# Optimization experiments

Measured on AMD Instinct MI355X. Metric: run time of the kernel, lower is better.

## Reference

```python
import jax, jax.numpy as jnp
import numpy as np

EPS = 1e-5
K_PATCHES = 5000  # sample_pixels // 16


def _resize_bilinear(x, h, w):
    # matches torch F.interpolate(mode='bilinear', align_corners=False)
    return jax.image.resize(x, (x.shape[0], x.shape[1], h, w), method="bilinear", antialias=False)


def _bn(x, g, b, m, v):
    # eval-mode BatchNorm2d with running stats
    inv = jax.lax.rsqrt(v + EPS)
    return (x - m[None, :, None, None]) * (g * inv)[None, :, None, None] + b[None, :, None, None]


def _conv(x, w):
    return jax.lax.conv_general_dilated(x, w, (1, 1), "VALID",
                                        dimension_numbers=("NCHW", "OIHW", "NCHW"))


def setup_inputs():
    key = jax.random.key(0)
    ks = jax.random.split(key, 14)
    B, Hc, Wc = 2, 512, 512
    pha = jax.random.uniform(ks[0], (B, 1, Hc, Wc), jnp.float32)
    err = jax.random.uniform(ks[1], (B, 1, Hc, Wc), jnp.float32)  # strictly >0 so mask is all-ones
    hid = jax.random.normal(ks[2], (B, 32, Hc, Wc), jnp.float32)

    def conv_w(k, o, i):
        return jax.random.normal(k, (o, i, 3, 3), jnp.float32) * 0.05

    def bn_p(k, c):
        k1, k2 = jax.random.split(k)
        return (1.0 + 0.1 * jax.random.normal(k1, (c,), jnp.float32),
                0.1 * jax.random.normal(k2, (c,), jnp.float32),
                jnp.zeros((c,), jnp.float32), jnp.ones((c,), jnp.float32))

    g1, b1, m1, v1 = bn_p(ks[4], 24)
    g2, b2, m2, v2 = bn_p(ks[6], 16)
    g3, b3, m3, v3 = bn_p(ks[8], 12)
    return dict(pha=pha, err=err, hid=hid,
                w1=conv_w(ks[3], 24, 33), g1=g1, b1=b1, m1=m1, v1=v1,
                w2=conv_w(ks[5], 16, 24), g2=g2, b2=b2, m2=m2, v2=v2,
                w3=conv_w(ks[7], 12, 16), g3=g3, b3=b3, m3=m3, v3=v3,
                w4=conv_w(ks[9], 1, 12),
                b4=0.1 * jax.random.normal(ks[10], (1,), jnp.float32),
                H_full=2048, W_full=2048)


def reference(pha, err, hid, w1, g1, b1, m1, v1, w2, g2, b2, m2, v2,
              w3, g3, b3, m3, v3, w4, b4, H_full, W_full):
    B = pha.shape[0]
    Hh, Wh = H_full // 2, W_full // 2
    Hq, Wq = H_full // 4, W_full // 4

    # --- select_refinement_regions (sampling mode) ---
    err_q = _resize_bilinear(err, Hq, Wq)                      # (B,1,Hq,Wq)
    flat = err_q.reshape(B, -1)
    _, top_idx = jax.lax.top_k(flat, K_PATCHES)                # (B,K)
    ref = jnp.zeros_like(flat).at[jnp.arange(B)[:, None], top_idx].set(1.0)
    ref = ref * (flat > 0).astype(flat.dtype)                  # prevent_oversampling
    ref = ref.reshape(B, 1, Hq, Wq)

    # nonzero(ref) == topk locations here (err is strictly positive)
    bidx = jnp.repeat(jnp.arange(B), K_PATCHES)                # (P,)
    hidx = (top_idx // Wq).reshape(-1)                         # (P,)
    widx = (top_idx % Wq).reshape(-1)                          # (P,)

    # --- crop_patch (unfold-equivalent gather), size=2, padding=3 ---
    x = jnp.concatenate([hid, pha], axis=1)                    # (B,33,Hc,Wc)
    x = _resize_bilinear(x, Hh, Wh)                            # (B,33,Hh,Wh)
    pad, size = 3, 2
    win = size + 2 * pad                                       # 8
    xp = jnp.pad(x, ((0, 0), (0, 0), (pad, pad), (pad, pad)))
    rows = hidx[:, None] * size + jnp.arange(win)              # (P,8)
    cols = widx[:, None] * size + jnp.arange(win)              # (P,8)
    patches = xp[bidx[:, None, None], :, rows[:, :, None], cols[:, None, :]]  # (P,8,8,33)
    patches = patches.transpose(0, 3, 1, 2)                    # (P,33,8,8)

    # --- small conv stack ---
    y = jax.nn.relu(_bn(_conv(patches, w1), g1, b1, m1, v1))   # (P,24,6,6)
    y = jax.nn.relu(_bn(_conv(y, w2), g2, b2, m2, v2))         # (P,16,4,4)
    y = jnp.repeat(jnp.repeat(y, 2, axis=2), 2, axis=3)        # nearest -> (P,16,8,8)
    y = jax.nn.relu(_bn(_conv(y, w3), g3, b3, m3, v3))         # (P,12,6,6)
    y = _conv(y, w4) + b4[None, :, None, None]                 # (P,1,4,4)

    # --- replace_patch (scatter_nd of 4x4 blocks into full-res pha) ---
    pha_full = _resize_bilinear(pha, H_full, W_full)           # (B,1,H,W)
    pr = hidx[:, None, None] * 4 + jnp.arange(4)[None, :, None]  # (P,4,1)
    pc = widx[:, None, None] * 4 + jnp.arange(4)[None, None, :]  # (P,1,4)
    pha_full = pha_full.at[bidx[:, None, None], 0, pr, pc].set(y[:, 0])
    return pha_full, ref
```

## Files before the change

### kernel.cpp

```cpp
#include <hip/hip_runtime.h>
#include <stdint.h>

#define K_SEL 5000
#define NQ    262144
#define NB    2

#define BIAS_OFF 38912
#define W4_OFF   39424
#define ST_OFF   40960
#define XT_OFF   135168
#define XT_BYTES ((size_t)NB * NQ * 40 * 2)
#define WS_NEED  (XT_OFF + XT_BYTES)

#define WS_HIST  16
#define WS_SEL   2064
#define WS_EQ    12064
#define EQ_CAP   4096
#define WS_BCNT  20480
#define WS_BBASE 21504

typedef _Float16 f16x8 __attribute__((ext_vector_type(8)));
typedef _Float16 f16x4 __attribute__((ext_vector_type(4)));
typedef float    f32x4 __attribute__((ext_vector_type(4)));
#define MFMA16(a,b,c) __builtin_amdgcn_mfma_f32_16x16x32_f16(a,b,c,0,0,0)

__global__ void prep_kernel(const float* __restrict__ w1, const float* __restrict__ g1,
                            const float* __restrict__ b1, const float* __restrict__ m1,
                            const float* __restrict__ v1,
                            const float* __restrict__ w2, const float* __restrict__ g2,
                            const float* __restrict__ b2, const float* __restrict__ m2,
                            const float* __restrict__ v2,
                            const float* __restrict__ w3, const float* __restrict__ g3,
                            const float* __restrict__ b3, const float* __restrict__ m3,
                            const float* __restrict__ v3,
                            const float* __restrict__ w4, const float* __restrict__ b4,
                            char* __restrict__ ws) {
    _Float16* wf = (_Float16*)ws;
    float* bias = (float*)(ws + BIAS_OFF);
    float* w4r  = (float*)(ws + W4_OFF);
    uint32_t* st = (uint32_t*)(ws + ST_OFF);
    int tid = threadIdx.x;
    for (int t = tid; t < 38 * 512; t += 256) {
        int frag = t >> 9, li = (t >> 3) & 63, j = t & 7;
        int lo = li & 15, hi = li >> 4;
        float val = 0.f;
        if (frag < 18) {
            int ky = frag / 6, r = frag % 6, kx = r >> 1, mt = r & 1;
            int oc = mt * 16 + lo, ci = hi * 8 + j;
            if (oc < 24) val = w1[((oc * 33 + ci) * 3 + ky) * 3 + kx] * g1[oc] * rsqrtf(v1[oc] + 1e-5f);
        } else if (frag < 27) {
            int f = frag - 18, ky = f / 3, kt = f % 3;
            int oc = lo, k = kt * 32 + hi * 8 + j;
            if (k < 72) {
                int kx = k / 24, ci = k % 24;
                val = w2[((oc * 24 + ci) * 3 + ky) * 3 + kx] * g2[oc] * rsqrtf(v2[oc] + 1e-5f);
            }
        } else if (frag < 36) {
            int s = frag - 27, ky = s / 3, kx = s % 3;
            int oc = lo, ci = hi * 8 + j;
            if (oc < 12 && ci < 16) val = w3[((oc * 16 + ci) * 3 + ky) * 3 + kx] * g3[oc] * rsqrtf(v3[oc] + 1e-5f);
        } else {
            int mt = frag - 36, oc = mt * 16 + lo, tap = hi * 8 + j;
            if (oc < 24 && tap < 9)
                val = w1[((oc * 33 + 32) * 3 + tap / 3) * 3 + tap % 3] * g1[oc] * rsqrtf(v1[oc] + 1e-5f);
        }
        wf[t] = (_Float16)val;
    }
    if (tid < 53) {
        float v;
        if (tid < 24)      { float sc = g1[tid] * rsqrtf(v1[tid] + 1e-5f); v = b1[tid] - m1[tid] * sc; }
        else if (tid < 40) { int c = tid - 24; float sc = g2[c] * rsqrtf(v2[c] + 1e-5f); v = b2[c] - m2[c] * sc; }
        else if (tid < 52) { int c = tid - 40; float sc = g3[c] * rsqrtf(v3[c] + 1e-5f); v = b3[c] - m3[c] * sc; }
        else v = b4[0];
        bias[tid] = v;
    }
    if (tid < 144) { int t9 = tid / 16, ci = tid % 16; w4r[tid] = (ci < 12) ? w4[ci * 9 + t9] : 0.f; }
    for (int i = tid; i < WS_HIST + 4 * 512; i += 256) st[i] = 0u;
    __syncthreads();
    if (tid == 0) { st[2] = K_SEL; st[3] = K_SEL; }
}

__device__ __forceinline__ void tu_work(int tb, const float* __restrict__ hid,
                                        const float* __restrict__ pha,
                                        _Float16* __restrict__ xt,
                                        float* __restrict__ out) {
    int tid = threadIdx.x;
    if (tb < 2048) {
        int t = tb * 256 + tid;
        int b = t >> 18, i = t & (NQ - 1);
        _Float16 v[40];
#pragma unroll
        for (int c = 0; c < 32; c++)
            v[c] = (_Float16)hid[((size_t)(b * 32 + c)) * NQ + i];
        v[32] = (_Float16)pha[(size_t)b * NQ + i];
#pragma unroll
        for (int c = 33; c < 40; c++) v[c] = (_Float16)0.f;
        _Float16* dst = xt + (size_t)t * 40;
#pragma unroll
        for (int q = 0; q < 5; q++) *(f16x8*)(dst + q * 8) = *(const f16x8*)(v + q * 8);
    } else {
        int t = (tb - 2048) * 256 + tid;
        int xq = t & 511;
        int rest = t >> 9;
        int oy = rest & 2047;
        int b  = rest >> 11;
        const float* src = pha + (size_t)b * NQ;
        float sy = oy * 0.25f - 0.375f;
        sy = fminf(fmaxf(sy, 0.0f), 511.0f);
        int y0 = (int)sy; int y1i = min(y0 + 1, 511);
        float fy = sy - (float)y0;
        float rv[4];
#pragma unroll
        for (int j = 0; j < 4; j++) {
            int ox = xq * 4 + j;
            float sx = ox * 0.25f - 0.375f;
            sx = fminf(fmaxf(sx, 0.0f), 511.0f);
            int x0 = (int)sx; int x1i = min(x0 + 1, 511);
            float fx = sx - (float)x0;
            float v00 = src[y0 * 512 + x0],  v01 = src[y0 * 512 + x1i];
            float v10 = src[y1i * 512 + x0], v11 = src[y1i * 512 + x1i];
            rv[j] = v00 * (1.f - fy) * (1.f - fx) + v01 * (1.f - fy) * fx
                  + v10 * fy * (1.f - fx)         + v11 * fy * fx;
        }
        float4 r4 = make_float4(rv[0], rv[1], rv[2], rv[3]);
        *reinterpret_cast<float4*>(out + (size_t)b * 4194304 + (size_t)oy * 2048 + xq * 4) = r4;
    }
}

__global__ void upsample_kernel(const float* __restrict__ pha, float* __restrict__ out) {
    int t = blockIdx.x * 256 + threadIdx.x;
    int xq = t & 511;
    int rest = t >> 9;
    int oy = rest & 2047;
    int b  = rest >> 11;
    const float* src = pha + (size_t)b * NQ;
    float sy = oy * 0.25f - 0.375f;
    sy = fminf(fmaxf(sy, 0.0f), 511.0f);
    int y0 = (int)sy; int y1i = min(y0 + 1, 511);
    float fy = sy - (float)y0;
    float rv[4];
#pragma unroll
    for (int j = 0; j < 4; j++) {
        int ox = xq * 4 + j;
        float sx = ox * 0.25f - 0.375f;
        sx = fminf(fmaxf(sx, 0.0f), 511.0f);
        int x0 = (int)sx; int x1i = min(x0 + 1, 511);
        float fx = sx - (float)x0;
        float v00 = src[y0 * 512 + x0],  v01 = src[y0 * 512 + x1i];
        float v10 = src[y1i * 512 + x0], v11 = src[y1i * 512 + x1i];
        rv[j] = v00 * (1.f - fy) * (1.f - fx) + v01 * (1.f - fy) * fx
              + v10 * fy * (1.f - fx)         + v11 * fy * fx;
    }
    float4 r4 = make_float4(rv[0], rv[1], rv[2], rv[3]);
    *reinterpret_cast<float4*>(out + (size_t)b * 4194304 + (size_t)oy * 2048 + xq * 4) = r4;
}

__global__ void hist_kernel(const float* __restrict__ err, uint32_t* st, int round,
                            const float* __restrict__ hid, const float* __restrict__ pha,
                            _Float16* __restrict__ xt, float* __restrict__ out, int tu_base) {
    if (blockIdx.x >= 2048) { tu_work(blockIdx.x - 2048 + tu_base, hid, pha, xt, out); return; }
    __shared__ uint32_t h[256];
    h[threadIdx.x] = 0u;
    __syncthreads();
    int t = blockIdx.x * 256 + threadIdx.x;
    int b = t >> 18;
    uint32_t bits = __float_as_uint(err[t]);
    uint32_t pref = st[b];
    int shift = 24 - 8 * round;
    bool match = (round == 0) || ((bits >> (shift + 8)) == (pref >> (shift + 8)));
    if (match) atomicAdd(&h[(bits >> shift) & 255u], 1u);
    __syncthreads();
    uint32_t v = h[threadIdx.x];
    if (v) atomicAdd(&st[WS_HIST + round * 512 + b * 256 + threadIdx.x], v);
}

__global__ void scan_kernel(uint32_t* st, int round) {
    int b = blockIdx.x;
    int lane = threadIdx.x;
    int shift = 24 - 8 * round;
    const uint32_t* hist = st + WS_HIST + round * 512 + b * 256;
    int binbase = 255 - 4 * lane;
    uint32_t hv0 = hist[binbase], hv1 = hist[binbase - 1],
             hv2 = hist[binbase - 2], hv3 = hist[binbase - 3];
    uint32_t p = hv0 + hv1 + hv2 + hv3;
    uint32_t cum = p;
    for (int o = 1; o < 64; o <<= 1) {
        uint32_t n = __shfl_up(cum, o);
        if (lane >= o) cum += n;
    }
    uint32_t rem = st[2 + b];
    unsigned long long bal = __ballot(cum >= rem);
    int first = __ffsll(bal) - 1;
    if (lane == first) {
        uint32_t acc = cum - p;
        uint32_t hv[4] = {hv0, hv1, hv2, hv3};
        int chosen = binbase;
        for (int q = 0; q < 4; q++) {
            if (acc + hv[q] >= rem) { chosen = binbase - q; break; }
            acc += hv[q];
        }
        uint32_t pref = st[b] | ((uint32_t)chosen << shift);
        st[b] = pref;
        st[2 + b] = rem - acc;
        if (round == 3) { st[4 + b] = pref; st[6 + b] = rem - acc; }
    }
}

__global__ void ccount_kernel(const float* __restrict__ err, uint32_t* st,
                              const float* __restrict__ hid, const float* __restrict__ pha,
                              _Float16* __restrict__ xt, float* __restrict__ out, int tu_base) {
    if (blockIdx.x >= 1024) { tu_work(blockIdx.x - 1024 + tu_base, hid, pha, xt, out); return; }
    __shared__ uint32_t wsum[8];
    int blk = blockIdx.x, tid = threadIdx.x;
    int b = blk >> 9, base = (blk & 511) << 9;
    uint32_t T = st[4 + b];
    uint32_t b0 = __float_as_uint(err[b * NQ + base + tid]);
    uint32_t b1 = __float_as_uint(err[b * NQ + base + 256 + tid]);
    unsigned long long m0 = __ballot(b0 > T);
    unsigned long long m1 = __ballot(b1 > T);
    int w = tid >> 6, lane = tid & 63;
    if (lane == 0) { wsum[w] = (uint32_t)__popcll(m0); wsum[4 + w] = (uint32_t)__popcll(m1); }
    __syncthreads();
    if (tid == 0)
        st[WS_BCNT + blk] = wsum[0] + wsum[1] + wsum[2] + wsum[3]
                          + wsum[4] + wsum[5] + wsum[6] + wsum[7];
}

__global__ void cscan_kernel(uint32_t* st) {
    __shared__ uint32_t wtot[8];
    int b = blockIdx.x, tid = threadIdx.x;
    int lane = tid & 63, w = tid >> 6;
    uint32_t v = st[WS_BCNT + b * 512 + tid];
    uint32_t inc = v;
    for (int o = 1; o < 64; o <<= 1) {
        uint32_t n = __shfl_up(inc, o);
        if (lane >= o) inc += n;
    }
    if (lane == 63) wtot[w] = inc;
    __syncthreads();
    uint32_t off = 0;
    for (int j = 0; j < w; j++) off += wtot[j];
    uint32_t base = off + inc - v;
    st[WS_BBASE + b * 512 + tid] = base;
    if (tid == 511) st[8 + b] = base + v;
}

__global__ void cplace_kernel(const float* __restrict__ err, uint32_t* st,
                              float* __restrict__ refout,
                              const float* __restrict__ hid, const float* __restrict__ pha,
                              _Float16* __restrict__ xt, float* __restrict__ out, int tu_base) {
    if (blockIdx.x >= 1024) { tu_work(blockIdx.x - 1024 + tu_base, hid, pha, xt, out); return; }
    __shared__ uint32_t wc[8];
    int blk = blockIdx.x, tid = threadIdx.x;
    int b = blk >> 9, base = (blk & 511) << 9;
    uint32_t T = st[4 + b];
    uint32_t blkbase = st[WS_BBASE + b * 512 + (blk & 511)];
    int i0 = base + tid, i1 = base + 256 + tid;
    uint32_t b0 = __float_as_uint(err[b * NQ + i0]);
    uint32_t b1 = __float_as_uint(err[b * NQ + i1]);
    bool s0 = b0 > T, s1 = b1 > T;
    unsigned long long m0 = __ballot(s0);
    unsigned long long m1 = __ballot(s1);
    int w = tid >> 6, lane = tid & 63;
    if (lane == 0) { wc[w] = (uint32_t)__popcll(m0); wc[4 + w] = (uint32_t)__popcll(m1); }
    refout[b * NQ + i0] = s0 ? 1.0f : 0.0f;
    refout[b * NQ + i1] = s1 ? 1.0f : 0.0f;
    __syncthreads();
    uint32_t tot0 = wc[0] + wc[1] + wc[2] + wc[3];
    uint32_t pre0 = 0, pre1 = tot0;
    for (int j = 0; j < w; j++) { pre0 += wc[j]; pre1 += wc[4 + j]; }
    unsigned long long lt = (1ull << lane) - 1ull;
    if (s0) {
        uint32_t slot = blkbase + pre0 + (uint32_t)__popcll(m0 & lt);
        if (slot < K_SEL) st[WS_SEL + b * K_SEL + slot] = (uint32_t)i0;
    }
    if (s1) {
        uint32_t slot = blkbase + pre1 + (uint32_t)__popcll(m1 & lt);
        if (slot < K_SEL) st[WS_SEL + b * K_SEL + slot] = (uint32_t)i1;
    }
    if (b0 == T) { uint32_t e = atomicAdd(&st[10 + b], 1u); if (e < EQ_CAP) st[WS_EQ + b * EQ_CAP + e] = (uint32_t)i0; }
    if (b1 == T) { uint32_t e = atomicAdd(&st[10 + b], 1u); if (e < EQ_CAP) st[WS_EQ + b * EQ_CAP + e] = (uint32_t)i1; }
}

__global__ void select_kernel(uint32_t* st, float* __restrict__ refout) {
    __shared__ uint32_t L[EQ_CAP];
    int b = blockIdx.x;
    uint32_t m = st[10 + b]; if (m > EQ_CAP) m = EQ_CAP;
    uint32_t need = st[6 + b];
    uint32_t T = st[4 + b];
    for (uint32_t j = threadIdx.x; j < m; j += blockDim.x) L[j] = st[WS_EQ + b * EQ_CAP + j];
    __syncthreads();
    for (uint32_t j = threadIdx.x; j < m; j += blockDim.x) {
        uint32_t idx = L[j];
        uint32_t rank = 0;
        for (uint32_t q = 0; q < m; q++) rank += (L[q] < idx) ? 1u : 0u;
        if (rank < need) {
            uint32_t slot = atomicAdd(&st[8 + b], 1u);
            if (slot < K_SEL) st[WS_SEL + b * K_SEL + slot] = idx;
            refout[b * NQ + idx] = (T != 0u) ? 1.0f : 0.0f;
        }
    }
}

__device__ __forceinline__ f16x8 ldfrag(const _Float16* wf, int frag, int l) {
    return *(const f16x8*)(wf + frag * 512 + l * 8);
}

template<bool XT>
__global__ __launch_bounds__(128) void patch_kernel(
    const float* __restrict__ hid, const float* __restrict__ pha,
    const _Float16* __restrict__ xt,
    const char* __restrict__ ws, float* __restrict__ out) {
    __shared__ _Float16 xs[64][40];
    __shared__ _Float16 y1n[36][40];
    __shared__ _Float16 pool[64][40];
    __shared__ float pha8[64];
    __shared__ float biasL[56];
    float* y3s = (float*)&y1n[0][0];

    const _Float16* wf = (const _Float16*)ws;
    const float* biasG = (const float*)(ws + BIAS_OFF);
    const float* w4r   = (const float*)(ws + W4_OFF);
    const uint32_t* st = (const uint32_t*)(ws + ST_OFF);

    int tid = threadIdx.x, l = tid & 63, wid = tid >> 6;
    int lo = l & 15, hi = l >> 4;
    int bp = blockIdx.x;
    int b = (bp >= K_SEL) ? 1 : 0;
    int pi = bp - b * K_SEL;
    uint32_t idx = st[WS_SEL + b * K_SEL + pi] & 0x3FFFFu;
    int hq = (int)(idx >> 9), wq = (int)(idx & 511u);

    if (tid < 53) biasL[tid] = biasG[tid];

    int ry = l >> 3, rx = l & 7;
    int hy = hq * 2 + ry - 3, hx = wq * 2 + rx - 3;
    bool inb = ((unsigned)hy < 1024u) && ((unsigned)hx < 1024u);
    float sy = fminf(fmaxf(hy * 0.5f - 0.25f, 0.f), 511.f);
    float sx = fminf(fmaxf(hx * 0.5f - 0.25f, 0.f), 511.f);
    int y0 = (int)sy, x0 = (int)sx;
    int y1c = min(y0 + 1, 511), x1c = min(x0 + 1, 511);
    float fy = sy - (float)y0, fx = sx - (float)x0;
    int o00 = y0 * 512 + x0, o01 = y0 * 512 + x1c, o10 = y1c * 512 + x0, o11 = y1c * 512 + x1c;
    float w00 = (1.f - fy) * (1.f - fx), w01 = (1.f - fy) * fx;
    float w10 = fy * (1.f - fx), w11 = fy * fx;

    _Float16 hv[16];
    if (XT) {
        if (inb) {
            const _Float16* xtb = xt + (size_t)b * NQ * 40 + (size_t)wid * 16;
            const _Float16* p00 = xtb + (size_t)o00 * 40;
            const _Float16* p01 = xtb + (size_t)o01 * 40;
            const _Float16* p10 = xtb + (size_t)o10 * 40;
            const _Float16* p11 = xtb + (size_t)o11 * 40;
            f16x8 a0 = *(const f16x8*)p00, a1 = *(const f16x8*)(p00 + 8);
            f16x8 b0 = *(const f16x8*)p01, b1 = *(const f16x8*)(p01 + 8);
            f16x8 c0 = *(const f16x8*)p10, c1 = *(const f16x8*)(p10 + 8);
            f16x8 d0 = *(const f16x8*)p11, d1 = *(const f16x8*)(p11 + 8);
#pragma unroll
            for (int j = 0; j < 8; j++) {
                hv[j]     = (_Float16)(w00 * (float)a0[j] + w01 * (float)b0[j]
                                     + w10 * (float)c0[j] + w11 * (float)d0[j]);
                hv[j + 8] = (_Float16)(w00 * (float)a1[j] + w01 * (float)b1[j]
                                     + w10 * (float)c1[j] + w11 * (float)d1[j]);
            }
        } else {
#pragma unroll
            for (int c = 0; c < 16; c++) hv[c] = (_Float16)0.f;
        }
    } else {
        const float* hb = hid + ((size_t)b * 32 + wid * 16) * NQ;
#pragma unroll
        for (int c = 0; c < 16; c++) {
            const float* p = hb + (size_t)c * NQ;
            float v = 0.f;
            if (inb) v = p[o00] * w00 + p[o01] * w01 + p[o10] * w10 + p[o11] * w11;
            hv[c] = (_Float16)v;
        }
    }
    f16x8 h0 = {hv[0], hv[1], hv[2], hv[3], hv[4], hv[5], hv[6], hv[7]};
    f16x8 h1 = {hv[8], hv[9], hv[10], hv[11], hv[12], hv[13], hv[14], hv[15]};
    {
        _Float16* xrow = &xs[l][wid * 16];
        *(f16x8*)xrow = h0;
        *((f16x8*)xrow + 1) = h1;
    }
    f16x8 z8 = {(_Float16)0.f, (_Float16)0.f, (_Float16)0.f, (_Float16)0.f,
                (_Float16)0.f, (_Float16)0.f, (_Float16)0.f, (_Float16)0.f};
    if (wid == 1) {
        const float* p = pha + (size_t)b * NQ;
        float v = 0.f;
        if (inb) v = p[o00] * w00 + p[o01] * w01 + p[o10] * w10 + p[o11] * w11;
        pha8[l] = v;
    }
    __syncthreads();

    if (wid == 0) {
        if (l < 48) {
            int py = (l * 43) >> 8, px = l - py * 6;
            _Float16 tap[9];
#pragma unroll
            for (int t = 0; t < 9; t++) {
                int ky = t / 3, kx = t % 3;
                int ip = (py + ky) * 8 + px + kx;
                tap[t] = (_Float16)pha8[ip & 63];
            }
            _Float16* row = &pool[l][0];
            f16x8 r0 = {tap[0], tap[1], tap[2], tap[3], tap[4], tap[5], tap[6], tap[7]};
            f16x8 r1 = z8; r1[0] = tap[8];
            *(f16x8*)row = r0;
            *(f16x8*)(row + 8)  = r1;
            *(f16x8*)(row + 16) = z8;
            *(f16x8*)(row + 24) = z8;
        }
    } else {
        for (int i = l; i < 72; i += 64) {
            *(f16x8*)&y1n[i >> 1][24 + (i & 1) * 8] = z8;
        }
    }
    __syncthreads();

    f32x4 zf = {0.f, 0.f, 0.f, 0.f};
    f32x4 aA0 = zf, aA1 = zf, aB = zf;
    int nA = wid * 16 + lo, nB = 32 + lo;
    int pyA = (nA * 43) >> 8, pxA = nA - pyA * 6;
    int pyB = (nB * 43) >> 8, pxB = nB - pyB * 6;
    {
        f16x8 A0 = ldfrag(wf, 36, l), A1 = ldfrag(wf, 37, l);
        f16x8 BA = *(const f16x8*)&pool[nA][hi * 8];
        f16x8 BB = *(const f16x8*)&pool[nB][hi * 8];
        aA0 = MFMA16(A0, BA, aA0);
        aA1 = MFMA16(A1, BA, aA1);
        aB  = MFMA16(wid ? A1 : A0, BB, aB);
    }
#pragma unroll
    for (int ky = 0; ky < 3; ky++) {
#pragma unroll
        for (int kt = 0; kt < 3; kt++) {
            f16x8 A0 = ldfrag(wf, ky * 6 + kt * 2 + 0, l);
            f16x8 A1 = ldfrag(wf, ky * 6 + kt * 2 + 1, l);
            int rA = ((pyA + ky) * 8 + pxA + kt) & 63;
            int rB = ((pyB + ky) * 8 + pxB + kt) & 63;
            f16x8 BA = *(const f16x8*)&xs[rA][hi * 8];
            f16x8 BB = *(const f16x8*)&xs[rB][hi * 8];
            aA0 = MFMA16(A0, BA, aA0);
            aA1 = MFMA16(A1, BA, aA1);
            aB  = MFMA16(wid ? A1 : A0, BB, aB);
        }
    }
    {
        f32x4 accs[3] = {aA0, aA1, aB};
        int mts[3] = {0, 1, wid};
        int nts[3] = {wid, wid, 2};
#pragma unroll
        for (int f = 0; f < 3; f++) {
            int n = nts[f] * 16 + lo;
            int ocb = mts[f] * 16 + hi * 4;
            if (n < 36 && ocb < 24) {
                f16x4 hh;
                hh[0] = (_Float16)fmaxf(accs[f][0] + biasL[ocb + 0], 0.f);
                hh[1] = (_Float16)fmaxf(accs[f][1] + biasL[ocb + 1], 0.f);
                hh[2] = (_Float16)fmaxf(accs[f][2] + biasL[ocb + 2], 0.f);
                hh[3] = (_Float16)fmaxf(accs[f][3] + biasL[ocb + 3], 0.f);
                *(f16x4*)&y1n[n][ocb] = hh;
            }
        }
    }
    __syncthreads();

    if (wid == 0) {
        f32x4 a2 = zf;
        int qy = lo >> 2, qx = lo & 3;
#pragma unroll
        for (int ky = 0; ky < 3; ky++) {
#pragma unroll
            for (int kt = 0; kt < 3; kt++) {
                f16x8 A = ldfrag(wf, 18 + ky * 3 + kt, l);
                int k = kt * 32 + hi * 8;
                const _Float16* bptr;
                if (k < 72) {
                    int kx = k / 24, ci0 = k - kx * 24;
                    bptr = &y1n[(qy + ky) * 6 + qx + kx][ci0];
                } else {
                    bptr = &y1n[0][24];
                }
                f16x8 B = *(const f16x8*)bptr;
                a2 = MFMA16(A, B, a2);
            }
        }
        int ocb = hi * 4;
        f16x4 hh;
        hh[0] = (_Float16)fmaxf(a2[0] + biasL[24 + ocb + 0], 0.f);
        hh[1] = (_Float16)fmaxf(a2[1] + biasL[24 + ocb + 1], 0.f);
        hh[2] = (_Float16)fmaxf(a2[2] + biasL[24 + ocb + 2], 0.f);
        hh[3] = (_Float16)fmaxf(a2[3] + biasL[24 + ocb + 3], 0.f);
#pragma unroll
        for (int dy = 0; dy < 2; dy++)
#pragma unroll
            for (int dx = 0; dx < 2; dx++) {
                int row = (2 * qy + dy) * 8 + 2 * qx + dx;
                *(f16x4*)&pool[row][ocb] = hh;
            }
    } else {
        *(f16x8*)&pool[l][16] = z8;
        *(f16x8*)&pool[l][24] = z8;
    }
    __syncthreads();

    f32x4 aC = zf, aD = zf;
    int nC = wid * 16 + lo, nD = 32 + lo;
    int pyC = (nC * 43) >> 8, pxC = nC - pyC * 6;
    int pyD = (nD * 43) >> 8, pxD = nD - pyD * 6;
#pragma unroll
    for (int s = 0; s < 9; s++) {
        int ky = s / 3, kx = s % 3;
        f16x8 A = ldfrag(wf, 27 + s, l);
        f16x8 BC = *(const f16x8*)&pool[((pyC + ky) * 8 + pxC + kx) & 63][hi * 8];
        aC = MFMA16(A, BC, aC);
        if (wid) {
            f16x8 BD = *(const f16x8*)&pool[((pyD + ky) * 8 + pxD + kx) & 63][hi * 8];
            aD = MFMA16(A, BD, aD);
        }
    }
    __syncthreads();
    {
        int ocb = hi * 4;
        f32x4 accs[2] = {aC, aD};
        int nts[2] = {wid, 2};
        int cnt = wid ? 2 : 1;
        for (int f = 0; f < cnt; f++) {
            int n = nts[f] * 16 + lo;
            if (n < 36) {
                f32x4 v;
#pragma unroll
                for (int r = 0; r < 4; r++) {
                    float bb = (ocb + r < 12) ? biasL[40 + ocb + r] : 0.f;
                    float x = accs[f][r] + bb;
                    v[r] = (ocb + r < 12) ? fmaxf(x, 0.f) : 0.f;
                }
                *(f32x4*)&y3s[n * 16 + ocb] = v;
            }
        }
    }
    __syncthreads();

    if (wid == 0) {
        int r4 = lo >> 2, c4 = lo & 3, cig = hi;
        float acc = 0.f;
#pragma unroll
        for (int t = 0; t < 9; t++) {
            int ky = t / 3, kx = t % 3;
            const f32x4 xv = *(const f32x4*)&y3s[((r4 + ky) * 6 + c4 + kx) * 16 + cig * 4];
            const f32x4 wv = *(const f32x4*)(w4r + t * 16 + cig * 4);
            acc += xv[0] * wv[0] + xv[1] * wv[1] + xv[2] * wv[2] + xv[3] * wv[3];
        }
        acc += __shfl_xor(acc, 32);
        acc += __shfl_xor(acc, 16);
        if (l < 16) {
            out[(size_t)b * 4194304 + (size_t)(hq * 4 + r4) * 2048 + (wq * 4 + c4)] = acc + biasL[52];
        }
    }
}

extern "C" void kernel_launch(void* const* d_in, const int* in_sizes, int n_in,
                              void* d_out, int out_size, void* d_ws, size_t ws_size,
                              hipStream_t stream) {
    const float* pha = (const float*)d_in[0];
    const float* err = (const float*)d_in[1];
    const float* hid = (const float*)d_in[2];
    const float* w1  = (const float*)d_in[3];
    const float* g1  = (const float*)d_in[4];
    const float* bb1 = (const float*)d_in[5];
    const float* m1  = (const float*)d_in[6];
    const float* v1  = (const float*)d_in[7];
    const float* w2  = (const float*)d_in[8];
    const float* g2  = (const float*)d_in[9];
    const float* bb2 = (const float*)d_in[10];
    const float* m2  = (const float*)d_in[11];
    const float* v2  = (const float*)d_in[12];
    const float* w3  = (const float*)d_in[13];
    const float* g3  = (const float*)d_in[14];
    const float* bb3 = (const float*)d_in[15];
    const float* m3  = (const float*)d_in[16];
    const float* v3  = (const float*)d_in[17];
    const float* w4  = (const float*)d_in[18];
    const float* b4  = (const float*)d_in[19];

    float* out    = (float*)d_out;
    float* refout = out + (size_t)NB * 4194304;
    char* ws      = (char*)d_ws;
    uint32_t* st  = (uint32_t*)(ws + ST_OFF);
    _Float16* xt  = (_Float16*)(ws + XT_OFF);
    bool use_xt   = (ws_size >= WS_NEED);

    prep_kernel<<<1, 256, 0, stream>>>(w1, g1, bb1, m1, v1, w2, g2, bb2, m2, v2,
                                       w3, g3, bb3, m3, v3, w4, b4, ws);
    if (use_xt) {
        const int NTU = 10240, SLICE = 1707;
        int off = 0;
        for (int r = 0; r < 4; r++) {
            int n = (off + SLICE <= NTU) ? SLICE : (NTU - off);
            hist_kernel<<<2048 + n, 256, 0, stream>>>(err, st, r, hid, pha, xt, out, off);
            off += n;
            scan_kernel<<<2, 64, 0, stream>>>(st, r);
        }
        {
            int n = (off + SLICE <= NTU) ? SLICE : (NTU - off);
            ccount_kernel<<<1024 + n, 256, 0, stream>>>(err, st, hid, pha, xt, out, off);
            off += n;
        }
        cscan_kernel<<<2, 512, 0, stream>>>(st);
        {
            int n = NTU - off;
            cplace_kernel<<<1024 + n, 256, 0, stream>>>(err, st, refout, hid, pha, xt, out, off);
        }
        select_kernel<<<2, 256, 0, stream>>>(st, refout);
        patch_kernel<true><<<2 * K_SEL, 128, 0, stream>>>(hid, pha, xt, ws, out);
    } else {
        upsample_kernel<<<8192, 256, 0, stream>>>(pha, out);
        for (int r = 0; r < 4; r++) {
            hist_kernel<<<2048, 256, 0, stream>>>(err, st, r, hid, pha, xt, out, 0);
            scan_kernel<<<2, 64, 0, stream>>>(st, r);
        }
        ccount_kernel<<<1024, 256, 0, stream>>>(err, st, hid, pha, xt, out, 0);
        cscan_kernel<<<2, 512, 0, stream>>>(st);
        cplace_kernel<<<1024, 256, 0, stream>>>(err, st, refout, hid, pha, xt, out, 0);
        select_kernel<<<2, 256, 0, stream>>>(st, refout);
        patch_kernel<false><<<2 * K_SEL, 128, 0, stream>>>(hid, pha, xt, ws, out);
    }
}
```

Baseline: 152.7 us.

## Fold radix-select scans into consumer kernels and parallelize prep

Removes the separate scan_kernel launches between radix histogram rounds and the cscan_kernel. Each consumer block now redundantly recomputes the prefix/remaining count from the stored histograms (chain_scan) or the block-base prefix sum via a reduction over block counts. Prep kernel is spread across 64 blocks instead of one. This cuts six tiny serialized launches and their gaps, at the cost of redundant per-block scan work and extra global histogram reads in every block.

```diff
diff --git a/kernel.cpp b/kernel.cpp
--- a/kernel.cpp
+++ b/kernel.cpp
@@ -17,7 +17,6 @@
 #define WS_EQ    12064
 #define EQ_CAP   4096
 #define WS_BCNT  20480
-#define WS_BBASE 21504
 
 typedef _Float16 f16x8 __attribute__((ext_vector_type(8)));
 typedef _Float16 f16x4 __attribute__((ext_vector_type(4)));
@@ -40,7 +39,7 @@
     float* w4r  = (float*)(ws + W4_OFF);
     uint32_t* st = (uint32_t*)(ws + ST_OFF);
     int tid = threadIdx.x;
-    for (int t = tid; t < 38 * 512; t += 256) {
+    for (int t = blockIdx.x * 256 + tid; t < 38 * 512; t += 64 * 256) {
         int frag = t >> 9, li = (t >> 3) & 63, j = t & 7;
         int lo = li & 15, hi = li >> 4;
         float val = 0.f;
@@ -66,18 +65,51 @@
         }
         wf[t] = (_Float16)val;
     }
-    if (tid < 53) {
-        float v;
-        if (tid < 24)      { float sc = g1[tid] * rsqrtf(v1[tid] + 1e-5f); v = b1[tid] - m1[tid] * sc; }
-        else if (tid < 40) { int c = tid - 24; float sc = g2[c] * rsqrtf(v2[c] + 1e-5f); v = b2[c] - m2[c] * sc; }
-        else if (tid < 52) { int c = tid - 40; float sc = g3[c] * rsqrtf(v3[c] + 1e-5f); v = b3[c] - m3[c] * sc; }
-        else v = b4[0];
-        bias[tid] = v;
-    }
-    if (tid < 144) { int t9 = tid / 16, ci = tid % 16; w4r[tid] = (ci < 12) ? w4[ci * 9 + t9] : 0.f; }
-    for (int i = tid; i < WS_HIST + 4 * 512; i += 256) st[i] = 0u;
-    __syncthreads();
-    if (tid == 0) { st[2] = K_SEL; st[3] = K_SEL; }
+    if (blockIdx.x == 0) {
+        if (tid < 53) {
+            float v;
+            if (tid < 24)      { float sc = g1[tid] * rsqrtf(v1[tid] + 1e-5f); v = b1[tid] - m1[tid] * sc; }
+            else if (tid < 40) { int c = tid - 24; float sc = g2[c] * rsqrtf(v2[c] + 1e-5f); v = b2[c] - m2[c] * sc; }
+            else if (tid < 52) { int c = tid - 40; float sc = g3[c] * rsqrtf(v3[c] + 1e-5f); v = b3[c] - m3[c] * sc; }
+            else v = b4[0];
+            bias[tid] = v;
+        }
+        if (tid < 144) { int t9 = tid / 16, ci = tid % 16; w4r[tid] = (ci < 12) ? w4[ci * 9 + t9] : 0.f; }
+        for (int i = tid; i < WS_HIST + 4 * 512; i += 256) st[i] = 0u;
+    }
+}
+
+__device__ __forceinline__ void chain_scan(const uint32_t* __restrict__ st, int b, int nrounds,
+                                           uint32_t* pref_out, uint32_t* rem_out) {
+    int lane = threadIdx.x & 63;
+    uint32_t pref = 0u, rem = K_SEL;
+    for (int r = 0; r < nrounds; r++) {
+        const uint32_t* hist = st + WS_HIST + r * 512 + b * 256;
+        int binbase = 255 - 4 * lane;
+        uint32_t hv0 = hist[binbase], hv1 = hist[binbase - 1],
+                 hv2 = hist[binbase - 2], hv3 = hist[binbase - 3];
+        uint32_t p = hv0 + hv1 + hv2 + hv3;
+        uint32_t cum = p;
+        for (int o = 1; o < 64; o <<= 1) {
+            uint32_t n = __shfl_up(cum, o);
+            if (lane >= o) cum += n;
+        }
+        unsigned long long bal = __ballot(cum >= rem);
+        int first = __ffsll(bal) - 1;
+        uint32_t acc = cum - p;
+        uint32_t hv[4] = {hv0, hv1, hv2, hv3};
+        int ch = binbase;
+        for (int q = 0; q < 4; q++) {
+            if (acc + hv[q] >= rem) { ch = binbase - q; break; }
+            acc += hv[q];
+        }
+        uint32_t chosen = (uint32_t)__shfl((int)ch, first);
+        uint32_t nrem   = (uint32_t)__shfl((int)(rem - acc), first);
+        pref |= chosen << (24 - 8 * r);
+        rem = nrem;
+    }
+    *pref_out = pref;
+    *rem_out = rem;
 }
 
 __device__ __forceinline__ void tu_work(int tb, const float* __restrict__ hid,
@@ -161,49 +193,18 @@
     if (blockIdx.x >= 2048) { tu_work(blockIdx.x - 2048 + tu_base, hid, pha, xt, out); return; }
     __shared__ uint32_t h[256];
     h[threadIdx.x] = 0u;
-    __syncthreads();
     int t = blockIdx.x * 256 + threadIdx.x;
     int b = t >> 18;
+    uint32_t pref = 0u, rem;
+    if (round > 0) chain_scan(st, b, round, &pref, &rem);
+    __syncthreads();
     uint32_t bits = __float_as_uint(err[t]);
-    uint32_t pref = st[b];
     int shift = 24 - 8 * round;
     bool match = (round == 0) || ((bits >> (shift + 8)) == (pref >> (shift + 8)));
     if (match) atomicAdd(&h[(bits >> shift) & 255u], 1u);
     __syncthreads();
     uint32_t v = h[threadIdx.x];
     if (v) atomicAdd(&st[WS_HIST + round * 512 + b * 256 + threadIdx.x], v);
-}
-
-__global__ void scan_kernel(uint32_t* st, int round) {
-    int b = blockIdx.x;
-    int lane = threadIdx.x;
-    int shift = 24 - 8 * round;
-    const uint32_t* hist = st + WS_HIST + round * 512 + b * 256;
-    int binbase = 255 - 4 * lane;
-    uint32_t hv0 = hist[binbase], hv1 = hist[binbase - 1],
-             hv2 = hist[binbase - 2], hv3 = hist[binbase - 3];
-    uint32_t p = hv0 + hv1 + hv2 + hv3;
-    uint32_t cum = p;
-    for (int o = 1; o < 64; o <<= 1) {
-        uint32_t n = __shfl_up(cum, o);
-        if (lane >= o) cum += n;
-    }
-    uint32_t rem = st[2 + b];
-    unsigned long long bal = __ballot(cum >= rem);
-    int first = __ffsll(bal) - 1;
-    if (lane == first) {
-        uint32_t acc = cum - p;
-        uint32_t hv[4] = {hv0, hv1, hv2, hv3};
-        int chosen = binbase;
-        for (int q = 0; q < 4; q++) {
-            if (acc + hv[q] >= rem) { chosen = binbase - q; break; }
-            acc += hv[q];
-        }
-        uint32_t pref = st[b] | ((uint32_t)chosen << shift);
-        st[b] = pref;
-        st[2 + b] = rem - acc;
-        if (round == 3) { st[4 + b] = pref; st[6 + b] = rem - acc; }
-    }
 }
 
 __global__ void ccount_kernel(const float* __restrict__ err, uint32_t* st,
@@ -213,7 +214,12 @@
     __shared__ uint32_t wsum[8];
     int blk = blockIdx.x, tid = threadIdx.x;
     int b = blk >> 9, base = (blk & 511) << 9;
-    uint32_t T = st[4 + b];
+    uint32_t T, need;
+    chain_scan(st, b, 4, &T, &need);
+    if ((blk & 511) == 0 && tid == 0) {
+        atomicExch(&st[4 + b], T);
+        atomicExch(&st[6 + b], need);
+    }
     uint32_t b0 = __float_as_uint(err[b * NQ + base + tid]);
     uint32_t b1 = __float_as_uint(err[b * NQ + base + 256 + tid]);
     unsigned long long m0 = __ballot(b0 > T);
@@ -226,42 +232,33 @@
                           + wsum[4] + wsum[5] + wsum[6] + wsum[7];
 }
 
-__global__ void cscan_kernel(uint32_t* st) {
-    __shared__ uint32_t wtot[8];
-    int b = blockIdx.x, tid = threadIdx.x;
-    int lane = tid & 63, w = tid >> 6;
-    uint32_t v = st[WS_BCNT + b * 512 + tid];
-    uint32_t inc = v;
-    for (int o = 1; o < 64; o <<= 1) {
-        uint32_t n = __shfl_up(inc, o);
-        if (lane >= o) inc += n;
-    }
-    if (lane == 63) wtot[w] = inc;
-    __syncthreads();
-    uint32_t off = 0;
-    for (int j = 0; j < w; j++) off += wtot[j];
-    uint32_t base = off + inc - v;
-    st[WS_BBASE + b * 512 + tid] = base;
-    if (tid == 511) st[8 + b] = base + v;
-}
-
 __global__ void cplace_kernel(const float* __restrict__ err, uint32_t* st,
                               float* __restrict__ refout,
                               const float* __restrict__ hid, const float* __restrict__ pha,
                               _Float16* __restrict__ xt, float* __restrict__ out, int tu_base) {
     if (blockIdx.x >= 1024) { tu_work(blockIdx.x - 1024 + tu_base, hid, pha, xt, out); return; }
     __shared__ uint32_t wc[8];
+    __shared__ uint32_t red[4];
     int blk = blockIdx.x, tid = threadIdx.x;
     int b = blk >> 9, base = (blk & 511) << 9;
+    int w = tid >> 6, lane = tid & 63;
     uint32_t T = st[4 + b];
-    uint32_t blkbase = st[WS_BBASE + b * 512 + (blk & 511)];
+    uint32_t myp = blk & 511;
+    uint32_t c0 = st[WS_BCNT + b * 512 + 2 * tid];
+    uint32_t c1 = st[WS_BCNT + b * 512 + 2 * tid + 1];
+    uint32_t v = (((uint32_t)(2 * tid) < myp) ? c0 : 0u) + (((uint32_t)(2 * tid + 1) < myp) ? c1 : 0u);
+    for (int o = 1; o < 64; o <<= 1) v += __shfl_xor(v, o);
+    if (lane == 0) red[w] = v;
+    __syncthreads();
+    uint32_t blkbase = red[0] + red[1] + red[2] + red[3];
+    if (myp == 511 && tid == 0)
+        atomicExch(&st[8 + b], blkbase + st[WS_BCNT + b * 512 + 511]);
     int i0 = base + tid, i1 = base + 256 + tid;
     uint32_t b0 = __float_as_uint(err[b * NQ + i0]);
     uint32_t b1 = __float_as_uint(err[b * NQ + i1]);
     bool s0 = b0 > T, s1 = b1 > T;
     unsigned long long m0 = __ballot(s0);
     unsigned long long m1 = __ballot(s1);
-    int w = tid >> 6, lane = tid & 63;
     if (lane == 0) { wc[w] = (uint32_t)__popcll(m0); wc[4 + w] = (uint32_t)__popcll(m1); }
     refout[b * NQ + i0] = s0 ? 1.0f : 0.0f;
     refout[b * NQ + i1] = s1 ? 1.0f : 0.0f;
@@ -593,8 +590,8 @@
     _Float16* xt  = (_Float16*)(ws + XT_OFF);
     bool use_xt   = (ws_size >= WS_NEED);
 
-    prep_kernel<<<1, 256, 0, stream>>>(w1, g1, bb1, m1, v1, w2, g2, bb2, m2, v2,
-                                       w3, g3, bb3, m3, v3, w4, b4, ws);
+    prep_kernel<<<64, 256, 0, stream>>>(w1, g1, bb1, m1, v1, w2, g2, bb2, m2, v2,
+                                        w3, g3, bb3, m3, v3, w4, b4, ws);
     if (use_xt) {
         const int NTU = 10240, SLICE = 1707;
         int off = 0;
@@ -602,14 +599,12 @@
             int n = (off + SLICE <= NTU) ? SLICE : (NTU - off);
             hist_kernel<<<2048 + n, 256, 0, stream>>>(err, st, r, hid, pha, xt, out, off);
             off += n;
-            scan_kernel<<<2, 64, 0, stream>>>(st, r);
         }
         {
             int n = (off + SLICE <= NTU) ? SLICE : (NTU - off);
             ccount_kernel<<<1024 + n, 256, 0, stream>>>(err, st, hid, pha, xt, out, off);
             off += n;
         }
-        cscan_kernel<<<2, 512, 0, stream>>>(st);
         {
             int n = NTU - off;
             cplace_kernel<<<1024 + n, 256, 0, stream>>>(err, st, refout, hid, pha, xt, out, off);
@@ -618,12 +613,9 @@
         patch_kernel<true><<<2 * K_SEL, 128, 0, stream>>>(hid, pha, xt, ws, out);
     } else {
         upsample_kernel<<<8192, 256, 0, stream>>>(pha, out);
-        for (int r = 0; r < 4; r++) {
+        for (int r = 0; r < 4; r++)
             hist_kernel<<<2048, 256, 0, stream>>>(err, st, r, hid, pha, xt, out, 0);
-            scan_kernel<<<2, 64, 0, stream>>>(st, r);
-        }
         ccount_kernel<<<1024, 256, 0, stream>>>(err, st, hid, pha, xt, out, 0);
-        cscan_kernel<<<2, 512, 0, stream>>>(st);
         cplace_kernel<<<1024, 256, 0, stream>>>(err, st, refout, hid, pha, xt, out, 0);
         select_kernel<<<2, 256, 0, stream>>>(st, refout);
         patch_kernel<false><<<2 * K_SEL, 128, 0, stream>>>(hid, pha, xt, ws, out);
```

Result: faster. 136.7 us (-10.5%).
